# Performance work log

Hardware: AMD Instinct MI355X
Metric: run time of the kernel (lower is better)

Reference implementation:

```python
import jax, jax.numpy as jnp
import numpy as np
from jax import lax

DIMS, IN_DIM, NW = 32, 32, 8
N, T, H, W = 8, 16, 112, 112
EPS = 1e-5

def setup_inputs() -> dict:
    key = jax.random.key(0)
    ks = jax.random.split(key, 12)
    fan = IN_DIM * 27
    inp = {
        'x': jax.random.normal(ks[0], (N, IN_DIM, T, H, W), jnp.float32),
        'std_x': jax.random.normal(ks[1], (N, 1, 32, 32), jnp.float32),
        'epochs_num': 5,
        'weights': jax.random.normal(ks[2], (NW, DIMS, IN_DIM, 3, 3, 3), jnp.float32) * np.sqrt(2.0 / fan),
        'biases': jax.random.normal(ks[3], (NW, DIMS), jnp.float32),
        'conv1_w': jax.random.normal(ks[4], (16, 1, 5, 5), jnp.float32) * 0.2,
        'conv1_b': jax.random.normal(ks[5], (16,), jnp.float32) * 0.1,
        'conv2_w': jax.random.normal(ks[6], (32, 16, 5, 5), jnp.float32) * 0.05,
        'conv2_b': jax.random.normal(ks[7], (32,), jnp.float32) * 0.1,
        'fc_w': jax.random.normal(ks[8], (NW, 32), jnp.float32) * 0.1,
        'fc_b': jax.random.normal(ks[9], (NW,), jnp.float32) * 0.1,
        'bn_gamma': jnp.ones((DIMS,), jnp.float32),
        'bn_beta': jnp.zeros((DIMS,), jnp.float32),
    }
    return inp

def _routing(std_x, c1w, c1b, c2w, c2b, fcw, fcb, tau):
    dn = ('NCHW', 'OIHW', 'NCHW')
    h = lax.conv_general_dilated(std_x, c1w, (1, 1), 'VALID', dimension_numbers=dn)
    h = jax.nn.relu(h + c1b[None, :, None, None])
    h = lax.conv_general_dilated(h, c2w, (1, 1), 'VALID', dimension_numbers=dn)
    h = jax.nn.relu(h + c2b[None, :, None, None])
    h = jnp.max(h, axis=(2, 3))                      # adaptive max pool to 1 -> [n,32]
    logits = h @ fcw.T + fcb                          # [n, num_weights]
    return jax.nn.softmax(logits / tau, axis=1)

def reference(x, std_x, epochs_num, weights, biases, conv1_w, conv1_b, conv2_w, conv2_b, fc_w, fc_b, bn_gamma, bn_beta):
    tau = 30.0 - 2.9 * epochs_num if epochs_num < 10 else 1.0
    phi = _routing(std_x, conv1_w, conv1_b, conv2_w, conv2_b, fc_w, fc_b, tau)
    dyn_w = jnp.einsum('bn,ncidhw->bcidhw', phi, weights)   # per-sample filters [n,dims,in,3,3,3]
    dyn_b = jnp.einsum('bn,nc->bc', phi, biases)            # [n,dims]
    dn3 = ('NCDHW', 'OIDHW', 'NCDHW')
    def per_sample(xi, wi):
        return lax.conv_general_dilated(xi[None], wi, (1, 1, 1), 'SAME', dimension_numbers=dn3)[0]
    y = jax.vmap(per_sample)(x, dyn_w)                      # [n,dims,T,H,W]
    y = y + dyn_b[:, :, None, None, None]
    # BatchNorm3d (training mode: batch stats, biased variance)
    mean = jnp.mean(y, axis=(0, 2, 3, 4))
    var = jnp.var(y, axis=(0, 2, 3, 4))
    y = (y - mean[None, :, None, None, None]) * lax.rsqrt(var + EPS)[None, :, None, None, None]
    y = y * bn_gamma[None, :, None, None, None] + bn_beta[None, :, None, None, None]
    return jax.nn.relu(y)
```

## Files before the change

kernel.cpp:

```cpp
#include <hip/hip_runtime.h>
#include <hip/hip_bf16.h>

#define IN_DIM 32
#define DIMS   32
#define NW     8
#define NB     8
#define TT     16
#define HH     112
#define WW     112
#define HW     (HH*WW)
#define CHW    (TT*HW)
#define EPS    1e-5f

typedef __attribute__((ext_vector_type(8))) short bf16x8;
typedef __attribute__((ext_vector_type(4))) float f32x4;

static __device__ __forceinline__ unsigned short f2bf(float f) {
    unsigned u = __float_as_uint(f);
    unsigned r = u + 0x7FFFu + ((u >> 16) & 1u);
    return (unsigned short)(r >> 16);
}

#define WSF_PHI    0
#define WSF_DYNB   64
#define WSF_STATS  320
#define WSF_HDR_FLOATS 448
#define XT_USHORTS  ((size_t)NB*CHW*32)
#define WS_NEED_BYTES (WSF_HDR_FLOATS*4 + (size_t)NB*27*1024*2 + XT_USHORTS*2)

#define WS_PHI    0
#define WS_DYNW   64
#define WS_DYNB   221248
#define WS_STATS  221504
#define WS_SS     221568

__global__ __launch_bounds__(256)
void routing_conv1_kernel(const float* __restrict__ std_x,
                          const float* __restrict__ c1w, const float* __restrict__ c1b,
                          float* __restrict__ h1g)
{
    const int oc = blockIdx.x, b = blockIdx.y;
    const int tid = threadIdx.x;
    __shared__ float sx[1024];
    for (int i = tid; i < 1024; i += 256) sx[i] = std_x[b * 1024 + i];
    __syncthreads();

    float wloc[25];
    #pragma unroll
    for (int k = 0; k < 25; ++k) wloc[k] = c1w[oc * 25 + k];
    const float bias = c1b[oc];

    for (int idx = tid; idx < 784; idx += 256) {
        int xw = idx % 28, xh = idx / 28;
        float s = bias;
        #pragma unroll
        for (int ky = 0; ky < 5; ++ky)
            #pragma unroll
            for (int kx = 0; kx < 5; ++kx)
                s = fmaf(sx[(xh + ky) * 32 + xw + kx], wloc[ky * 5 + kx], s);
        h1g[(b * 16 + oc) * 784 + idx] = fmaxf(s, 0.f);
    }
}

__global__ __launch_bounds__(256)
void routing_conv2max_kernel(const float* __restrict__ h1g,
                             const float* __restrict__ c2w, const float* __restrict__ c2b,
                             float* __restrict__ cmax)
{
    const int oc = blockIdx.x, b = blockIdx.y;
    const int tid = threadIdx.x;
    __shared__ float h1s[16 * 784];
    __shared__ float wred[4];

    for (int i = tid; i < 16 * 784; i += 256) h1s[i] = h1g[b * (16 * 784) + i];
    __syncthreads();

    float m = 0.f;
    for (int idx = tid; idx < 576; idx += 256) {
        int xw = idx % 24, xh = idx / 24;
        float s = c2b[oc];
        for (int ic = 0; ic < 16; ++ic) {
            const float* hp = &h1s[ic * 784];
            const float* wp = &c2w[(oc * 16 + ic) * 25];
            #pragma unroll
            for (int ky = 0; ky < 5; ++ky)
                #pragma unroll
                for (int kx = 0; kx < 5; ++kx)
                    s = fmaf(hp[(xh + ky) * 28 + xw + kx], wp[ky * 5 + kx], s);
        }
        m = fmaxf(m, s);
    }
    #pragma unroll
    for (int off = 32; off >= 1; off >>= 1) m = fmaxf(m, __shfl_down(m, off));
    if ((tid & 63) == 0) wred[tid >> 6] = m;
    __syncthreads();
    if (tid == 0) {
        float r = fmaxf(fmaxf(wred[0], wred[1]), fmaxf(wred[2], wred[3]));
        cmax[b * 32 + oc] = r;
    }
}

__global__ __launch_bounds__(64)
void routing_fc_kernel(const float* __restrict__ cmax, const int* __restrict__ epochs,
                       const float* __restrict__ fcw, const float* __restrict__ fcb,
                       float* __restrict__ phi_out)
{
    const int tid = threadIdx.x;
    const int b = tid >> 3, n = tid & 7;
    int ep = epochs[0];
    float tau = (ep < 10) ? (30.0f - 2.9f * (float)ep) : 1.0f;
    float s = fcb[n];
    #pragma unroll
    for (int k = 0; k < 32; ++k) s = fmaf(cmax[b * 32 + k], fcw[n * 32 + k], s);
    s /= tau;
    float mx = s;
    #pragma unroll
    for (int off = 1; off < 8; off <<= 1) mx = fmaxf(mx, __shfl_xor(mx, off, 8));
    float e = expf(s - mx);
    float den = e;
    #pragma unroll
    for (int off = 1; off < 8; off <<= 1) den += __shfl_xor(den, off, 8);
    phi_out[b * 8 + n] = e / den;
}

#define XS 232
__global__ __launch_bounds__(256)
void xpose_kernel(const float* __restrict__ x, unsigned short* __restrict__ xT)
{
    const int h = blockIdx.x, t = blockIdx.y, b = blockIdx.z;
    const int tid = threadIdx.x;
    __shared__ __align__(16) unsigned char lds[32 * XS];

    for (int idx = tid; idx < 32 * 112; idx += 256) {
        int ic = idx / 112;
        int w = idx - ic * 112;
        float v = x[(((size_t)(b * 32 + ic) * TT + t) * HW) + h * 112 + w];
        *(unsigned short*)(lds + ic * XS + w * 2) = f2bf(v);
    }
    __syncthreads();

    unsigned short* op = xT + ((((size_t)b * TT + t) * HH + h) * WW) * 32;
    for (int idx = tid; idx < 448; idx += 256) {
        int w = idx >> 2, icg = idx & 3;
        unsigned int pk[4];
        #pragma unroll
        for (int j = 0; j < 4; ++j) {
            unsigned short lo = *(unsigned short*)(lds + (icg * 8 + 2 * j) * XS + w * 2);
            unsigned short hi = *(unsigned short*)(lds + (icg * 8 + 2 * j + 1) * XS + w * 2);
            pk[j] = (unsigned int)lo | ((unsigned int)hi << 16);
        }
        uint4 v; v.x = pk[0]; v.y = pk[1]; v.z = pk[2]; v.w = pk[3];
        *(uint4*)(op + (size_t)w * 32 + icg * 8) = v;
    }
}

__global__ __launch_bounds__(256)
void dynwb_kernel(const float* __restrict__ phi, const float* __restrict__ weights,
                  const float* __restrict__ biases, unsigned short* __restrict__ dwb,
                  float* __restrict__ dyn_b, float* __restrict__ stats)
{
    const int tap = blockIdx.x;
    const int b   = blockIdx.y;
    const int tid = threadIdx.x;
    __shared__ float ph[8];
    if (tid < 8) ph[tid] = phi[b * 8 + tid];
    __syncthreads();

    for (int e = tid; e < 1024; e += 256) {
        int oc = e >> 5, ic = e & 31;
        float s = 0.f;
        #pragma unroll
        for (int n = 0; n < 8; ++n)
            s = fmaf(ph[n], weights[(((size_t)n * 32 + oc) * 32 + ic) * 27 + tap], s);
        dwb[((size_t)(b * 27 + tap) << 10) + e] = f2bf(s);
    }
    if (tap == 0) {
        if (tid < 32) {
            float s = 0.f;
            #pragma unroll
            for (int n = 0; n < 8; ++n) s = fmaf(ph[n], biases[n * 32 + tid], s);
            dyn_b[b * 32 + tid] = s;
        }
        if (b == 0 && tid >= 64 && tid < 128) stats[tid - 64] = 0.f;
    }
}

#define ROWSTRIDE (18 * 64)
#define PLANE_BYTES (18 * ROWSTRIDE)
__global__ __launch_bounds__(256, 3)
void convmf_kernel(const unsigned short* __restrict__ xT, const unsigned short* __restrict__ dwb,
                   const float* __restrict__ dyn_b, float* __restrict__ y,
                   float* __restrict__ stats)
{
    const int hblk = blockIdx.x / 7, wblk = blockIdx.x % 7;
    const int tpair = blockIdx.y, b = blockIdx.z;
    const int h0 = hblk * 16, w0 = wblk * 16, t0 = tpair * 2;
    const int tid = threadIdx.x;
    const int lane = tid & 63, wv = tid >> 6;
    const int l15 = lane & 15, lg = lane >> 4;

    __shared__ __align__(16) unsigned char ldsx[2 * PLANE_BYTES];
    __shared__ float sred[64];

    f32x4 acc0[4][2], acc1[4][2];
    #pragma unroll
    for (int g = 0; g < 4; ++g)
        #pragma unroll
        for (int M = 0; M < 2; ++M) { acc0[g][M] = (f32x4)0.f; acc1[g][M] = (f32x4)0.f; }

    const unsigned short* wbase = dwb + (size_t)b * 27 * 1024;

    for (int tp = 0; tp < 4; ++tp) {
        {
            const int tx = t0 - 1 + tp;
            unsigned char* ldsp = ldsx + (tp & 1) * PLANE_BYTES;
            const bool tok = (unsigned)tx < (unsigned)TT;
            for (int cid = tid; cid < 1296; cid += 256) {
                int hr = cid / 72;
                int rem = cid - hr * 72;
                int p = rem >> 2, icg = rem & 3;
                int gh = h0 - 1 + hr, gw = w0 - 1 + p;
                uint4 v; v.x = 0; v.y = 0; v.z = 0; v.w = 0;
                if (tok && (unsigned)gh < (unsigned)HH && (unsigned)gw < (unsigned)WW)
                    v = *(const uint4*)(xT + ((((size_t)b * TT + tx) * HH + gh) * WW + gw) * 32 + icg * 8);
                *(uint4*)(ldsp + hr * ROWSTRIDE + p * 64 + icg * 16) = v;
            }
        }
        __syncthreads();

        const bool do0 = (tp <= 2), do1 = (tp >= 1);
        const int dt0 = tp, dt1 = tp - 1;
        const unsigned char* ldsp = ldsx + (tp & 1) * PLANE_BYTES;

        #pragma unroll
        for (int dhw = 0; dhw < 9; ++dhw) {
            const int dh = dhw / 3, dw = dhw - dh * 3;
            bf16x8 a00, a01, a10, a11;
            if (do0) {
                const unsigned short* wp = wbase + (dt0 * 9 + dhw) * 1024 + l15 * 32 + lg * 8;
                a00 = *(const bf16x8*)(wp);
                a01 = *(const bf16x8*)(wp + 512);
            }
            if (do1) {
                const unsigned short* wp = wbase + (dt1 * 9 + dhw) * 1024 + l15 * 32 + lg * 8;
                a10 = *(const bf16x8*)(wp);
                a11 = *(const bf16x8*)(wp + 512);
            }
            const unsigned char* bb0 = ldsp + (wv * 4 + dh) * ROWSTRIDE + (l15 + dw) * 64 + lg * 16;
            #pragma unroll
            for (int g = 0; g < 4; ++g) {
                bf16x8 bb = *(const bf16x8*)(bb0 + g * ROWSTRIDE);
                if (do0) {
                    acc0[g][0] = __builtin_amdgcn_mfma_f32_16x16x32_bf16(a00, bb, acc0[g][0], 0, 0, 0);
                    acc0[g][1] = __builtin_amdgcn_mfma_f32_16x16x32_bf16(a01, bb, acc0[g][1], 0, 0, 0);
                }
                if (do1) {
                    acc1[g][0] = __builtin_amdgcn_mfma_f32_16x16x32_bf16(a10, bb, acc1[g][0], 0, 0, 0);
                    acc1[g][1] = __builtin_amdgcn_mfma_f32_16x16x32_bf16(a11, bb, acc1[g][1], 0, 0, 0);
                }
            }
        }
        __syncthreads();
    }

    f32x4 bias[2];
    #pragma unroll
    for (int M = 0; M < 2; ++M)
        #pragma unroll
        for (int r = 0; r < 4; ++r)
            bias[M][r] = dyn_b[b * 32 + 16 * M + lg * 4 + r];

    float sumv[2][4], sqv[2][4];
    #pragma unroll
    for (int M = 0; M < 2; ++M)
        #pragma unroll
        for (int r = 0; r < 4; ++r) { sumv[M][r] = 0.f; sqv[M][r] = 0.f; }

    #pragma unroll
    for (int g = 0; g < 4; ++g) {
        const int h = h0 + wv * 4 + g;
        #pragma unroll
        for (int M = 0; M < 2; ++M) {
            f32x4 v0 = acc0[g][M] + bias[M];
            f32x4 v1 = acc1[g][M] + bias[M];
            const int oc0 = 16 * M + lg * 4;
            size_t base = (((size_t)(b * 32 + oc0) * TT + t0) * HW) + h * 112 + w0 + l15;
            #pragma unroll
            for (int r = 0; r < 4; ++r) {
                sumv[M][r] += v0[r] + v1[r];
                sqv[M][r]  += v0[r] * v0[r] + v1[r] * v1[r];
                y[base + (size_t)r * TT * HW] = v0[r];
                y[base + (size_t)r * TT * HW + HW] = v1[r];
            }
        }
    }

    #pragma unroll
    for (int off = 1; off < 16; off <<= 1) {
        #pragma unroll
        for (int M = 0; M < 2; ++M)
            #pragma unroll
            for (int r = 0; r < 4; ++r) {
                sumv[M][r] += __shfl_xor(sumv[M][r], off);
                sqv[M][r]  += __shfl_xor(sqv[M][r], off);
            }
    }
    if (tid < 64) sred[tid] = 0.f;
    __syncthreads();
    if (l15 == 0) {
        #pragma unroll
        for (int M = 0; M < 2; ++M)
            #pragma unroll
            for (int r = 0; r < 4; ++r) {
                int ch = 16 * M + lg * 4 + r;
                atomicAdd(&sred[ch], sumv[M][r]);
                atomicAdd(&sred[32 + ch], sqv[M][r]);
            }
    }
    __syncthreads();
    if (tid < 64) atomicAdd(&stats[tid], sred[tid]);
}

__global__ __launch_bounds__(256)
void norm_relu_fused_kernel(float* __restrict__ y, const float* __restrict__ stats,
                            const float* __restrict__ gamma, const float* __restrict__ beta)
{
    __shared__ float ssc[32], ssh[32];
    if (threadIdx.x < 32) {
        int c = threadIdx.x;
        const float M = (float)NB * (float)CHW;
        float mean = stats[c] / M;
        float var  = stats[32 + c] / M - mean * mean;
        float sc = gamma[c] * rsqrtf(var + EPS);
        ssc[c] = sc;
        ssh[c] = beta[c] - mean * sc;
    }
    __syncthreads();

    const long long total4 = (long long)NB * DIMS * CHW / 4;
    const int nthreads = gridDim.x * blockDim.x;
    float4* y4 = reinterpret_cast<float4*>(y);
    for (long long i = (long long)blockIdx.x * blockDim.x + threadIdx.x; i < total4; i += nthreads) {
        int c = (int)((i / (CHW / 4)) & 31);
        float sc = ssc[c];
        float sh = ssh[c];
        float4 v = y4[i];
        v.x = fmaxf(fmaf(v.x, sc, sh), 0.f);
        v.y = fmaxf(fmaf(v.y, sc, sh), 0.f);
        v.z = fmaxf(fmaf(v.z, sc, sh), 0.f);
        v.w = fmaxf(fmaf(v.w, sc, sh), 0.f);
        y4[i] = v;
    }
}

__global__ __launch_bounds__(256)
void routing_kernel(const float* __restrict__ std_x, const int* __restrict__ epochs,
                    const float* __restrict__ c1w, const float* __restrict__ c1b,
                    const float* __restrict__ c2w, const float* __restrict__ c2b,
                    const float* __restrict__ fcw, const float* __restrict__ fcb,
                    float* __restrict__ phi_out)
{
    const int b = blockIdx.x;
    const int tid = threadIdx.x;
    __shared__ float sx[32 * 32];
    __shared__ float h1[16 * 28 * 28];
    __shared__ float cmax[32];

    for (int i = tid; i < 1024; i += 256) sx[i] = std_x[b * 1024 + i];
    if (tid < 32) cmax[tid] = 0.f;
    __syncthreads();

    for (int idx = tid; idx < 16 * 28 * 28; idx += 256) {
        int xw = idx % 28;
        int r = idx / 28;
        int xh = r % 28;
        int oc = r / 28;
        float s = c1b[oc];
        #pragma unroll
        for (int ky = 0; ky < 5; ++ky)
            #pragma unroll
            for (int kx = 0; kx < 5; ++kx)
                s = fmaf(sx[(xh + ky) * 32 + xw + kx], c1w[oc * 25 + ky * 5 + kx], s);
        h1[idx] = fmaxf(s, 0.f);
    }
    __syncthreads();

    for (int idx = tid; idx < 32 * 24 * 24; idx += 256) {
        int xw = idx % 24;
        int r = idx / 24;
        int xh = r % 24;
        int oc = r / 24;
        float s = c2b[oc];
        for (int ic = 0; ic < 16; ++ic) {
            const float* hp = &h1[ic * 784];
            const float* wp = &c2w[(oc * 16 + ic) * 25];
            #pragma unroll
            for (int ky = 0; ky < 5; ++ky)
                #pragma unroll
                for (int kx = 0; kx < 5; ++kx)
                    s = fmaf(hp[(xh + ky) * 28 + xw + kx], wp[ky * 5 + kx], s);
        }
        s = fmaxf(s, 0.f);
        atomicMax(reinterpret_cast<int*>(&cmax[oc]), __float_as_int(s));
    }
    __syncthreads();

    if (tid == 0) {
        int ep = epochs[0];
        float tau = (ep < 10) ? (30.0f - 2.9f * (float)ep) : 1.0f;
        float lg[8];
        float mx = -1e30f;
        #pragma unroll
        for (int n = 0; n < 8; ++n) {
            float s = fcb[n];
            #pragma unroll
            for (int k = 0; k < 32; ++k) s = fmaf(cmax[k], fcw[n * 32 + k], s);
            lg[n] = s / tau;
            mx = fmaxf(mx, lg[n]);
        }
        float den = 0.f;
        #pragma unroll
        for (int n = 0; n < 8; ++n) { lg[n] = expf(lg[n] - mx); den += lg[n]; }
        #pragma unroll
        for (int n = 0; n < 8; ++n) phi_out[b * 8 + n] = lg[n] / den;
    }
}

__global__ __launch_bounds__(256)
void dynw_kernel(const float* __restrict__ phi, const float* __restrict__ weights,
                 const float* __restrict__ biases, float* __restrict__ dyn_w,
                 float* __restrict__ dyn_b, float* __restrict__ stats)
{
    const int b = blockIdx.x;
    const int tid = threadIdx.x;
    __shared__ float ph[8];
    if (tid < 8) ph[tid] = phi[b * 8 + tid];
    __syncthreads();

    for (int j = tid; j < DIMS * IN_DIM * 27; j += 256) {
        float s = 0.f;
        #pragma unroll
        for (int n = 0; n < 8; ++n) s = fmaf(ph[n], weights[n * (DIMS * IN_DIM * 27) + j], s);
        dyn_w[b * (DIMS * IN_DIM * 27) + j] = s;
    }
    if (tid < 32) {
        float s = 0.f;
        #pragma unroll
        for (int n = 0; n < 8; ++n) s = fmaf(ph[n], biases[n * 32 + tid], s);
        dyn_b[b * 32 + tid] = s;
    }
    if (b == 0 && tid < 64) stats[tid] = 0.f;
}

__global__ __launch_bounds__(256)
void conv3d_kernel(const float* __restrict__ x, const float* __restrict__ dyn_w,
                   const float* __restrict__ dyn_b, float* __restrict__ y,
                   float* __restrict__ stats)
{
    const int htile = blockIdx.x;
    const int t     = blockIdx.y;
    const int b     = blockIdx.z;
    const int tid   = threadIdx.x;
    const int w     = tid & 127;
    const int hh    = tid >> 7;
    const int h0    = htile * 2;

    __shared__ float tile[3][8][4][114];

    float acc[32];
    #pragma unroll
    for (int c = 0; c < 32; ++c) acc[c] = 0.f;

    const float* wb = dyn_w + b * (DIMS * IN_DIM * 27);
    const float* xb = x + (size_t)b * IN_DIM * CHW;

    for (int ic0 = 0; ic0 < 32; ic0 += 8) {
        __syncthreads();
        for (int idx = tid; idx < 3 * 8 * 4 * 114; idx += 256) {
            int w_ = idx % 114;
            int r  = idx / 114;
            int h_ = r & 3;
            int r2 = r >> 2;
            int i_ = r2 & 7;
            int dt_ = r2 >> 3;
            int gt = t + dt_ - 1;
            int gh = h0 - 1 + h_;
            int gw = w_ - 1;
            float v = 0.f;
            if ((unsigned)gt < (unsigned)TT && (unsigned)gh < (unsigned)HH && (unsigned)gw < (unsigned)WW)
                v = xb[(size_t)((ic0 + i_) * TT + gt) * HW + gh * WW + gw];
            tile[dt_][i_][h_][w_] = v;
        }
        __syncthreads();

        if (w < WW) {
            for (int i = 0; i < 8; ++i) {
                #pragma unroll
                for (int dt = 0; dt < 3; ++dt) {
                    float xv[9];
                    #pragma unroll
                    for (int dh = 0; dh < 3; ++dh)
                        #pragma unroll
                        for (int dw = 0; dw < 3; ++dw)
                            xv[dh * 3 + dw] = tile[dt][i][hh + dh][w + dw];
                    const float* wp = wb + (ic0 + i) * 27 + dt * 9;
                    #pragma unroll
                    for (int c = 0; c < 32; ++c) {
                        const float* wc = wp + c * 864;
                        #pragma unroll
                        for (int k = 0; k < 9; ++k)
                            acc[c] = fmaf(xv[k], wc[k], acc[c]);
                    }
                }
            }
        }
    }

    const float* db = dyn_b + b * 32;
    if (w < WW) {
        #pragma unroll
        for (int c = 0; c < 32; ++c) acc[c] += db[c];
    }

    __shared__ float ssum[32], ssq[32];
    if (tid < 32) { ssum[tid] = 0.f; ssq[tid] = 0.f; }
    __syncthreads();
    #pragma unroll
    for (int c = 0; c < 32; ++c) {
        float s = (w < WW) ? acc[c] : 0.f;
        float q = s * s;
        #pragma unroll
        for (int off = 32; off >= 1; off >>= 1) {
            s += __shfl_down(s, off);
            q += __shfl_down(q, off);
        }
        if ((tid & 63) == 0) { atomicAdd(&ssum[c], s); atomicAdd(&ssq[c], q); }
    }
    __syncthreads();
    if (tid < 32) {
        atomicAdd(&stats[tid], ssum[tid]);
        atomicAdd(&stats[32 + tid], ssq[tid]);
    }

    if (w < WW) {
        size_t base = ((size_t)(b * 32) * TT + t) * HW + (size_t)(h0 + hh) * WW + w;
        #pragma unroll
        for (int c = 0; c < 32; ++c)
            y[base + (size_t)c * CHW] = acc[c];
    }
}

__global__ void stats_finalize_kernel(const float* __restrict__ stats,
                                      const float* __restrict__ gamma,
                                      const float* __restrict__ beta,
                                      float* __restrict__ scaleshift)
{
    int c = threadIdx.x;
    const float M = (float)NB * (float)CHW;
    float mean = stats[c] / M;
    float var  = stats[32 + c] / M - mean * mean;
    float sc = gamma[c] * rsqrtf(var + EPS);
    scaleshift[c] = sc;
    scaleshift[32 + c] = beta[c] - mean * sc;
}

__global__ __launch_bounds__(256)
void norm_relu_kernel(float* __restrict__ y, const float* __restrict__ scaleshift)
{
    const long long total4 = (long long)NB * DIMS * CHW / 4;
    const int nthreads = gridDim.x * blockDim.x;
    float4* y4 = reinterpret_cast<float4*>(y);
    for (long long i = (long long)blockIdx.x * blockDim.x + threadIdx.x; i < total4; i += nthreads) {
        int c = (int)((i / (CHW / 4)) & 31);
        float sc = scaleshift[c];
        float sh = scaleshift[32 + c];
        float4 v = y4[i];
        v.x = fmaxf(fmaf(v.x, sc, sh), 0.f);
        v.y = fmaxf(fmaf(v.y, sc, sh), 0.f);
        v.z = fmaxf(fmaf(v.z, sc, sh), 0.f);
        v.w = fmaxf(fmaf(v.w, sc, sh), 0.f);
        y4[i] = v;
    }
}

extern "C" void kernel_launch(void* const* d_in, const int* in_sizes, int n_in,
                              void* d_out, int out_size, void* d_ws, size_t ws_size,
                              hipStream_t stream)
{
    const float* x      = (const float*)d_in[0];
    const float* std_x  = (const float*)d_in[1];
    const int*   epochs = (const int*)d_in[2];
    const float* weights= (const float*)d_in[3];
    const float* biases = (const float*)d_in[4];
    const float* c1w    = (const float*)d_in[5];
    const float* c1b    = (const float*)d_in[6];
    const float* c2w    = (const float*)d_in[7];
    const float* c2b    = (const float*)d_in[8];
    const float* fcw    = (const float*)d_in[9];
    const float* fcb    = (const float*)d_in[10];
    const float* gamma  = (const float*)d_in[11];
    const float* beta   = (const float*)d_in[12];

    float* out = (float*)d_out;
    float* ws  = (float*)d_ws;

    if (ws_size >= WS_NEED_BYTES) {
        float* phi   = ws + WSF_PHI;
        float* dyn_b = ws + WSF_DYNB;
        float* stats = ws + WSF_STATS;
        unsigned short* dwb = (unsigned short*)(ws + WSF_HDR_FLOATS);
        unsigned short* xT  = dwb + (size_t)NB * 27 * 1024;
        float* h1g  = (float*)xT;
        float* cmax = h1g + NB * 16 * 784;

        routing_conv1_kernel<<<dim3(16, NB), 256, 0, stream>>>(std_x, c1w, c1b, h1g);
        routing_conv2max_kernel<<<dim3(32, NB), 256, 0, stream>>>(h1g, c2w, c2b, cmax);
        routing_fc_kernel<<<1, 64, 0, stream>>>(cmax, epochs, fcw, fcb, phi);
        dynwb_kernel<<<dim3(27, NB), 256, 0, stream>>>(phi, weights, biases, dwb, dyn_b, stats);
        xpose_kernel<<<dim3(HH, TT, NB), 256, 0, stream>>>(x, xT);
        convmf_kernel<<<dim3(49, 8, NB), 256, 0, stream>>>(xT, dwb, dyn_b, out, stats);
        norm_relu_fused_kernel<<<2048, 256, 0, stream>>>(out, stats, gamma, beta);
    } else {
        float* phi   = ws + WS_PHI;
        float* dyn_w = ws + WS_DYNW;
        float* dyn_b = ws + WS_DYNB;
        float* stats = ws + WS_STATS;
        float* ss    = ws + WS_SS;

        routing_kernel<<<NB, 256, 0, stream>>>(std_x, epochs, c1w, c1b, c2w, c2b, fcw, fcb, phi);
        dynw_kernel<<<NB, 256, 0, stream>>>(phi, weights, biases, dyn_w, dyn_b, stats);
        conv3d_kernel<<<dim3(HH / 2, TT, NB), 256, 0, stream>>>(x, dyn_w, dyn_b, out, stats);
        stats_finalize_kernel<<<1, 32, 0, stream>>>(stats, gamma, beta, ss);
        norm_relu_kernel<<<2048, 256, 0, stream>>>(out, ss);
    }
}
```

Measured before the change: 682.0 us.

## Prefetch conv input planes via async global-to-LDS loads with double buffering

The conv kernel now stages each time plane into LDS with direct global_load_lds instructions, using precomputed per-thread addresses and a zero buffer for padding. The next plane is issued after the current plane's MFMA work, so loads overlap compute across the double buffer. The transpose kernel reads x as float4, dynwb is reorganised per output channel for coalesced weight reads, and LDS atomics for stats become per-wave slots. This adds a contiguous wave-level LDS layout and the assumption that the zero region (stats plus the zero slot) is cleared before use.

```diff
diff --git a/kernel.cpp b/kernel.cpp
--- a/kernel.cpp
+++ b/kernel.cpp
@@ -21,9 +21,17 @@
     return (unsigned short)(r >> 16);
 }
 
+static __device__ __forceinline__ void gload_lds16(const void* gptr, void* lptr) {
+    __builtin_amdgcn_global_load_lds(
+        (const __attribute__((address_space(1))) unsigned int*)gptr,
+        (__attribute__((address_space(3))) unsigned int*)lptr,
+        16, 0, 0);
+}
+
 #define WSF_PHI    0
 #define WSF_DYNB   64
 #define WSF_STATS  320
+#define WSF_ZERO   384
 #define WSF_HDR_FLOATS 448
 #define XT_USHORTS  ((size_t)NB*CHW*32)
 #define WS_NEED_BYTES (WSF_HDR_FLOATS*4 + (size_t)NB*27*1024*2 + XT_USHORTS*2)
@@ -131,11 +139,14 @@
     const int tid = threadIdx.x;
     __shared__ __align__(16) unsigned char lds[32 * XS];
 
-    for (int idx = tid; idx < 32 * 112; idx += 256) {
-        int ic = idx / 112;
-        int w = idx - ic * 112;
-        float v = x[(((size_t)(b * 32 + ic) * TT + t) * HW) + h * 112 + w];
-        *(unsigned short*)(lds + ic * XS + w * 2) = f2bf(v);
+    for (int idx = tid; idx < 32 * 28; idx += 256) {
+        int ic = idx / 28;
+        int w4 = idx - ic * 28;
+        const float4 v = *(const float4*)(x + (((size_t)(b * 32 + ic) * TT + t) * HW) + h * 112 + w4 * 4);
+        uint2 pk;
+        pk.x = (unsigned)f2bf(v.x) | ((unsigned)f2bf(v.y) << 16);
+        pk.y = (unsigned)f2bf(v.z) | ((unsigned)f2bf(v.w) << 16);
+        *(uint2*)(lds + ic * XS + w4 * 8) = pk;
     }
     __syncthreads();
 
@@ -157,40 +168,41 @@
 __global__ __launch_bounds__(256)
 void dynwb_kernel(const float* __restrict__ phi, const float* __restrict__ weights,
                   const float* __restrict__ biases, unsigned short* __restrict__ dwb,
-                  float* __restrict__ dyn_b, float* __restrict__ stats)
-{
-    const int tap = blockIdx.x;
-    const int b   = blockIdx.y;
+                  float* __restrict__ dyn_b, float* __restrict__ statszero)
+{
+    const int oc = blockIdx.x;
+    const int b  = blockIdx.y;
     const int tid = threadIdx.x;
     __shared__ float ph[8];
     if (tid < 8) ph[tid] = phi[b * 8 + tid];
     __syncthreads();
 
-    for (int e = tid; e < 1024; e += 256) {
-        int oc = e >> 5, ic = e & 31;
+    for (int i = tid; i < 864; i += 256) {
         float s = 0.f;
         #pragma unroll
         for (int n = 0; n < 8; ++n)
-            s = fmaf(ph[n], weights[(((size_t)n * 32 + oc) * 32 + ic) * 27 + tap], s);
-        dwb[((size_t)(b * 27 + tap) << 10) + e] = f2bf(s);
-    }
-    if (tap == 0) {
-        if (tid < 32) {
-            float s = 0.f;
-            #pragma unroll
-            for (int n = 0; n < 8; ++n) s = fmaf(ph[n], biases[n * 32 + tid], s);
-            dyn_b[b * 32 + tid] = s;
-        }
-        if (b == 0 && tid >= 64 && tid < 128) stats[tid - 64] = 0.f;
-    }
-}
-
-#define ROWSTRIDE (18 * 64)
-#define PLANE_BYTES (18 * ROWSTRIDE)
+            s = fmaf(ph[n], weights[(size_t)(n * 32 + oc) * 864 + i], s);
+        int ic = i / 27;
+        int tap = i - 27 * ic;
+        dwb[((size_t)(b * 27 + tap) << 10) + (oc << 5) + ic] = f2bf(s);
+    }
+    if (tid == 0) {
+        float s = 0.f;
+        #pragma unroll
+        for (int n = 0; n < 8; ++n) s = fmaf(ph[n], biases[n * 32 + oc], s);
+        dyn_b[b * 32 + oc] = s;
+    }
+    if (oc == 0 && b == 0 && tid < 128) statszero[tid] = 0.f;
+}
+
+#define ROWSTRIDE   (18 * 64)
+#define CELLS       1296
+#define BUF_BYTES   (1536 * 16)
+#define PLANE_BYTES_G 802816ull
 __global__ __launch_bounds__(256, 3)
 void convmf_kernel(const unsigned short* __restrict__ xT, const unsigned short* __restrict__ dwb,
-                   const float* __restrict__ dyn_b, float* __restrict__ y,
-                   float* __restrict__ stats)
+                   const float* __restrict__ dyn_b, const float* __restrict__ zerobuf,
+                   float* __restrict__ y, float* __restrict__ stats)
 {
     const int hblk = blockIdx.x / 7, wblk = blockIdx.x % 7;
     const int tpair = blockIdx.y, b = blockIdx.z;
@@ -199,8 +211,35 @@
     const int lane = tid & 63, wv = tid >> 6;
     const int l15 = lane & 15, lg = lane >> 4;
 
-    __shared__ __align__(16) unsigned char ldsx[2 * PLANE_BYTES];
-    __shared__ float sred[64];
+    __shared__ __align__(16) unsigned char ldsx[2 * BUF_BYTES];
+    __shared__ float sred[4][64];
+
+    const unsigned char* xTbase = (const unsigned char*)xT + (size_t)b * TT * PLANE_BYTES_G;
+    const unsigned char* zbp = (const unsigned char*)zerobuf;
+    const unsigned char* cb[6];
+    bool okhw[6];
+    #pragma unroll
+    for (int j = 0; j < 6; ++j) {
+        int cid = j * 256 + tid;
+        int hr = cid / 72, rem = cid - hr * 72;
+        int p = rem >> 2, icg = rem & 3;
+        int gh = h0 - 1 + hr, gw = w0 - 1 + p;
+        okhw[j] = (cid < CELLS) && ((unsigned)gh < (unsigned)HH) && ((unsigned)gw < (unsigned)WW);
+        cb[j] = xTbase + (ptrdiff_t)(gh * WW + gw) * 64 + icg * 16;
+    }
+    unsigned char* lwave = ldsx + (size_t)(tid & ~63) * 16;
+
+#define STAGE(TX, SEL) do {                                                   \
+        const int tx_ = (TX);                                                 \
+        const bool tok_ = ((unsigned)tx_ < (unsigned)TT);                     \
+        const size_t toff_ = (size_t)tx_ * PLANE_BYTES_G;                     \
+        unsigned char* lb_ = lwave + (SEL) * BUF_BYTES;                       \
+        _Pragma("unroll")                                                     \
+        for (int j = 0; j < 6; ++j) {                                         \
+            const unsigned char* s_ = (tok_ && okhw[j]) ? cb[j] + toff_ : zbp;\
+            gload_lds16(s_, lb_ + j * 4096);                                  \
+        }                                                                     \
+    } while (0)
 
     f32x4 acc0[4][2], acc1[4][2];
     #pragma unroll
@@ -210,27 +249,15 @@
 
     const unsigned short* wbase = dwb + (size_t)b * 27 * 1024;
 
+    STAGE(t0 - 1, 0);
+    asm volatile("s_waitcnt vmcnt(0)" ::: "memory");
+    __syncthreads();
+
+    #pragma unroll
     for (int tp = 0; tp < 4; ++tp) {
-        {
-            const int tx = t0 - 1 + tp;
-            unsigned char* ldsp = ldsx + (tp & 1) * PLANE_BYTES;
-            const bool tok = (unsigned)tx < (unsigned)TT;
-            for (int cid = tid; cid < 1296; cid += 256) {
-                int hr = cid / 72;
-                int rem = cid - hr * 72;
-                int p = rem >> 2, icg = rem & 3;
-                int gh = h0 - 1 + hr, gw = w0 - 1 + p;
-                uint4 v; v.x = 0; v.y = 0; v.z = 0; v.w = 0;
-                if (tok && (unsigned)gh < (unsigned)HH && (unsigned)gw < (unsigned)WW)
-                    v = *(const uint4*)(xT + ((((size_t)b * TT + tx) * HH + gh) * WW + gw) * 32 + icg * 8);
-                *(uint4*)(ldsp + hr * ROWSTRIDE + p * 64 + icg * 16) = v;
-            }
-        }
-        __syncthreads();
-
         const bool do0 = (tp <= 2), do1 = (tp >= 1);
         const int dt0 = tp, dt1 = tp - 1;
-        const unsigned char* ldsp = ldsx + (tp & 1) * PLANE_BYTES;
+        const unsigned char* ldsp = ldsx + (tp & 1) * BUF_BYTES;
 
         #pragma unroll
         for (int dhw = 0; dhw < 9; ++dhw) {
@@ -260,8 +287,13 @@
                 }
             }
         }
+
+        if (tp < 3) STAGE(t0 + tp, (tp + 1) & 1);
+
+        asm volatile("s_waitcnt vmcnt(0)" ::: "memory");
         __syncthreads();
     }
+#undef STAGE
 
     f32x4 bias[2];
     #pragma unroll
@@ -305,20 +337,21 @@
                 sqv[M][r]  += __shfl_xor(sqv[M][r], off);
             }
     }
-    if (tid < 64) sred[tid] = 0.f;
-    __syncthreads();
     if (l15 == 0) {
         #pragma unroll
         for (int M = 0; M < 2; ++M)
             #pragma unroll
             for (int r = 0; r < 4; ++r) {
                 int ch = 16 * M + lg * 4 + r;
-                atomicAdd(&sred[ch], sumv[M][r]);
-                atomicAdd(&sred[32 + ch], sqv[M][r]);
+                sred[wv][ch] = sumv[M][r];
+                sred[wv][32 + ch] = sqv[M][r];
             }
     }
     __syncthreads();
-    if (tid < 64) atomicAdd(&stats[tid], sred[tid]);
+    if (tid < 64) {
+        float v = sred[0][tid] + sred[1][tid] + sred[2][tid] + sred[3][tid];
+        atomicAdd(&stats[tid], v);
+    }
 }
 
 __global__ __launch_bounds__(256)
@@ -608,6 +641,7 @@
         float* phi   = ws + WSF_PHI;
         float* dyn_b = ws + WSF_DYNB;
         float* stats = ws + WSF_STATS;
+        float* zerob = ws + WSF_ZERO;
         unsigned short* dwb = (unsigned short*)(ws + WSF_HDR_FLOATS);
         unsigned short* xT  = dwb + (size_t)NB * 27 * 1024;
         float* h1g  = (float*)xT;
@@ -616,9 +650,9 @@
         routing_conv1_kernel<<<dim3(16, NB), 256, 0, stream>>>(std_x, c1w, c1b, h1g);
         routing_conv2max_kernel<<<dim3(32, NB), 256, 0, stream>>>(h1g, c2w, c2b, cmax);
         routing_fc_kernel<<<1, 64, 0, stream>>>(cmax, epochs, fcw, fcb, phi);
-        dynwb_kernel<<<dim3(27, NB), 256, 0, stream>>>(phi, weights, biases, dwb, dyn_b, stats);
+        dynwb_kernel<<<dim3(32, NB), 256, 0, stream>>>(phi, weights, biases, dwb, dyn_b, stats);
         xpose_kernel<<<dim3(HH, TT, NB), 256, 0, stream>>>(x, xT);
-        convmf_kernel<<<dim3(49, 8, NB), 256, 0, stream>>>(xT, dwb, dyn_b, out, stats);
+        convmf_kernel<<<dim3(49, 8, NB), 256, 0, stream>>>(xT, dwb, dyn_b, zerob, out, stats);
         norm_relu_fused_kernel<<<2048, 256, 0, stream>>>(out, stats, gamma, beta);
     } else {
         float* phi   = ws + WS_PHI;
```

After: 634.1 us. 1.08x faster.
